# Kernel optimization log

Hardware: AMD Instinct MI355X
Metric: run time of the kernel (lower is better)

## Reference

```python
import jax, jax.numpy as jnp
import numpy as np

N = 50000      # num nodes
E = 400000     # num edges
D = 384        # input_dim
H = 4          # heads
C = 128        # hidden_dim per head
HC = H * C     # 512


def setup_inputs() -> dict:
    key = jax.random.key(0)
    ks = jax.random.split(key, 32)
    w = lambda k, shape: jax.random.normal(k, shape, jnp.float32) * 0.05
    inp = {
        "x": jax.random.normal(ks[0], (N, D), jnp.float32),
        "edge_index": jax.random.randint(ks[1], (2, E), 0, N, dtype=jnp.int32),
    }
    dims = [(D, HC), (HC, HC)]  # layer0 in=384, layer1 in=512
    i = 2
    for l, (din, dout) in enumerate(dims):
        for nm in ["q", "k", "v", "s"]:  # query/key/value/skip linears
            inp[f"{nm}{l}_w"] = w(ks[i], (dout, din)); i += 1
            inp[f"{nm}{l}_b"] = jnp.zeros((dout,), jnp.float32)
    inp["out_w"] = w(ks[i], (D, HC))
    inp["out_b"] = jnp.zeros((D,), jnp.float32)
    return inp


def _transformer_conv(x, src, dst, Wq, bq, Wk, bk, Wv, bv, Ws, bs):
    # PyG TransformerConv, concat=True, root_weight=True, no edge features.
    n = x.shape[0]
    q = (x @ Wq.T + bq).reshape(n, H, C)
    k = (x @ Wk.T + bk).reshape(n, H, C)
    v = (x @ Wv.T + bv).reshape(n, H, C)
    # per-edge attention logits [E, H]; target = dst, source = src
    alpha = (q[dst] * k[src]).sum(-1) / jnp.sqrt(jnp.float32(C))
    m = jax.ops.segment_max(alpha, dst, num_segments=n)
    m = jnp.where(jnp.isfinite(m), m, 0.0)  # nodes with no in-edges
    e = jnp.exp(alpha - m[dst])
    denom = jax.ops.segment_sum(e, dst, num_segments=n)
    a = e / (denom[dst] + 1e-16)             # segment softmax [E, H]
    msg = v[src] * a[:, :, None]             # [E, H, C]
    agg = jax.ops.segment_sum(msg, dst, num_segments=n).reshape(n, HC)
    return agg + x @ Ws.T + bs               # + root/skip connection


def reference(x, edge_index,
              q0_w, q0_b, k0_w, k0_b, v0_w, v0_b, s0_w, s0_b,
              q1_w, q1_b, k1_w, k1_b, v1_w, v1_b, s1_w, s1_b,
              out_w, out_b):
    src, dst = edge_index[0], edge_index[1]
    h = _transformer_conv(x, src, dst, q0_w, q0_b, k0_w, k0_b, v0_w, v0_b, s0_w, s0_b)
    h = jax.nn.relu(h)
    h = _transformer_conv(h, src, dst, q1_w, q1_b, k1_w, k1_b, v1_w, v1_b, s1_w, s1_b)
    h = jax.nn.relu(h)
    return h @ out_w.T + out_b  # [N, D]
```

## Files before the change

kernel.cpp:

```cpp
#include <hip/hip_runtime.h>
#include <hip/hip_bf16.h>

#define NN 50000
#define NE 400000
#define DD 384
#define HC 512

typedef unsigned int u32;
typedef unsigned short u16;
typedef __attribute__((ext_vector_type(8))) short bf16x8;
typedef __attribute__((ext_vector_type(4))) float f32x4;

#define AS1 __attribute__((address_space(1)))
#define AS3 __attribute__((address_space(3)))

__device__ __forceinline__ float bflo(u32 u){ return __uint_as_float(u << 16); }
__device__ __forceinline__ float bfhi(u32 u){ return __uint_as_float(u & 0xFFFF0000u); }
__device__ __forceinline__ u16 f2bf(float f){
    u32 u = __float_as_uint(f);
    return (u16)((u + 0x7FFFu + ((u >> 16) & 1u)) >> 16);
}
__device__ __forceinline__ u32 pack2(float a, float b){
    return (u32)f2bf(a) | ((u32)f2bf(b) << 16);
}
__device__ __forceinline__ float dot8(const float* q, uint4 k){
    return q[0] * bflo(k.x) + q[1] * bfhi(k.x)
         + q[2] * bflo(k.y) + q[3] * bfhi(k.y)
         + q[4] * bflo(k.z) + q[5] * bfhi(k.z)
         + q[6] * bflo(k.w) + q[7] * bfhi(k.w);
}

template<int K>
__global__ __launch_bounds__(512)
void gemm_ws(const u16* __restrict__ Ab, const u16* __restrict__ Wb,
             const float* __restrict__ bias,
             u16* __restrict__ oQ, u16* __restrict__ oK,
             u16* __restrict__ oV, u16* __restrict__ oS)
{
    constexpr int NKT  = K / 64;
    constexpr int WCH  = K / 8;
    constexpr int NPAN = (NN + 127) / 128;
    __shared__ char smW[128 * K * 2];
    __shared__ char smA[2][16384];

    const int b   = blockIdx.x;
    const int xcd = b & 7;
    const int idx = b >> 3;
    const int ct  = idx & 15;
    const int rh  = idx >> 4;

    const int tid  = threadIdx.x;
    const int lane = tid & 63;
    const int w    = tid >> 6;
    const int wq   = w >> 1;
    const int wc   = w & 1;
    const int r16  = lane & 15;
    const int kq   = lane >> 4;

    const u16* Wrow0 = Wb + (size_t)ct * 128 * K;
    #pragma unroll
    for (int p = 0; p < (128 * WCH) / 512; ++p) {
        int ci = p * 512 + tid;
        int row = ci / WCH, pc = ci % WCH;
        int lc = (pc & ~7) | ((pc ^ row) & 7);
        __builtin_amdgcn_global_load_lds((const AS1 u32*)(Wrow0 + (size_t)row * K + lc * 8),
                                         (AS3 u32*)(smW + (size_t)ci * 16), 16, 0, 0);
    }

    auto panel = [&](int j) { return (2 * j + rh) * 8 + xcd; };
    int np = 0;
    while (panel(np) < NPAN) ++np;
    const int total = np * NKT;

    auto stageA = [&](int t) {
        int j = t / NKT, kc = t - (t / NKT) * NKT;
        int m0 = panel(j) * 128;
        #pragma unroll
        for (int p = 0; p < 2; ++p) {
            int ci = p * 512 + tid;
            int row = ci >> 3, pc = ci & 7;
            int lc = pc ^ (row & 7);
            int gr = m0 + row; if (gr >= NN) gr = NN - 1;
            __builtin_amdgcn_global_load_lds((const AS1 u32*)(Ab + (size_t)gr * K + kc * 64 + lc * 8),
                                             (AS3 u32*)(smA[t & 1] + ci * 16), 16, 0, 0);
        }
    };

    stageA(0);
    stageA(1);

    f32x4 acc[2][4] = {};

    const int qsel = ct >> 2;
    u16* outp = (qsel == 0) ? oQ : (qsel == 1) ? oK : (qsel == 2) ? oV : oS;
    const int cb = (ct & 3) * 128 + wc * 64;
    float bv4[4];
    #pragma unroll
    for (int ni = 0; ni < 4; ++ni) bv4[ni] = bias[ct * 128 + wc * 64 + ni * 16 + r16];

    for (int t = 0; t < total; ++t) {
        if (t + 1 < total) { asm volatile("s_waitcnt vmcnt(2)" ::: "memory"); }
        else               { asm volatile("s_waitcnt vmcnt(0)" ::: "memory"); }
        __builtin_amdgcn_s_barrier();
        __builtin_amdgcn_sched_barrier(0);

        const int jj = t / NKT;
        const int kt = t - jj * NKT;
        const char* bufA = smA[t & 1];
        #pragma unroll
        for (int kk = 0; kk < 2; ++kk) {
            bf16x8 av[2], bv[4];
            #pragma unroll
            for (int i = 0; i < 2; ++i) {
                int rowA = wq * 32 + i * 16 + r16;
                int c = kk * 4 + kq;
                av[i] = *(const bf16x8*)(bufA + rowA * 128 + ((c ^ (rowA & 7)) << 4));
            }
            #pragma unroll
            for (int i = 0; i < 4; ++i) {
                int rowW = wc * 64 + i * 16 + r16;
                int c = kt * 8 + kk * 4 + kq;
                int pcw = (c & ~7) | ((c ^ rowW) & 7);
                bv[i] = *(const bf16x8*)(smW + (size_t)rowW * (K * 2) + (pcw << 4));
            }
            #pragma unroll
            for (int mi = 0; mi < 2; ++mi)
                #pragma unroll
                for (int ni = 0; ni < 4; ++ni)
                    acc[mi][ni] = __builtin_amdgcn_mfma_f32_16x16x32_bf16(
                        av[mi], bv[ni], acc[mi][ni], 0, 0, 0);
        }

        __builtin_amdgcn_sched_barrier(0);
        __builtin_amdgcn_s_barrier();
        __builtin_amdgcn_sched_barrier(0);

        if (kt == NKT - 1) {
            int m0 = panel(jj) * 128;
            #pragma unroll
            for (int ni = 0; ni < 4; ++ni) {
                int col = cb + ni * 16 + r16;
                float bb = bv4[ni];
                #pragma unroll
                for (int mi = 0; mi < 2; ++mi)
                    #pragma unroll
                    for (int r = 0; r < 4; ++r) {
                        int gr = m0 + wq * 32 + mi * 16 + kq * 4 + r;
                        if (gr < NN) outp[(size_t)gr * 512 + col] = f2bf(acc[mi][ni][r] + bb);
                        acc[mi][ni][r] = 0.f;
                    }
            }
        }
        if (t + 2 < total) stageA(t + 2);
    }
}

template<int K>
__global__ __launch_bounds__(256)
void gemm2ph(const u16* __restrict__ Ab, const u16* __restrict__ Wb,
             const float* __restrict__ bias, float* __restrict__ oF,
             int n, int Ototal, int NT)
{
    constexpr int NKT = K / 64;
    __shared__ char smA[2][16384];
    __shared__ char smB[2][16384];

    const int nb  = gridDim.x;
    const int bd  = blockIdx.x;
    const int q8  = nb >> 3, r8 = nb & 7;
    const int xcd = bd & 7, gg = bd >> 3;
    const int tt  = (xcd < r8 ? xcd * (q8 + 1) : r8 * (q8 + 1) + (xcd - r8) * q8) + gg;
    const int m0  = (tt / NT) * 128;
    const int o0  = (tt % NT) * 128;

    const int tid  = threadIdx.x;
    const int lane = tid & 63;
    const int w    = tid >> 6;
    const int wr   = w >> 1, wc = w & 1;
    const int r16  = lane & 15;
    const int kq   = lane >> 4;
    const int swz  = (r16 & 7) << 4;

    auto stage = [&](int bf, int kt) {
        #pragma unroll
        for (int p = 0; p < 4; ++p) {
            int ci = p * 256 + tid, row = ci >> 3, pc = ci & 7;
            int lc = pc ^ (row & 7);
            const u16* g = Wb + (size_t)(o0 + row) * K + kt * 64 + lc * 8;
            __builtin_amdgcn_global_load_lds((const AS1 u32*)g,
                                             (AS3 u32*)(smB[bf] + ci * 16), 16, 0, 0);
        }
        #pragma unroll
        for (int p = 0; p < 4; ++p) {
            int ci = p * 256 + tid, row = ci >> 3, pc = ci & 7;
            int lc = pc ^ (row & 7);
            int gr = m0 + row; if (gr >= n) gr = n - 1;
            const u16* g = Ab + (size_t)gr * K + kt * 64 + lc * 8;
            __builtin_amdgcn_global_load_lds((const AS1 u32*)g,
                                             (AS3 u32*)(smA[bf] + ci * 16), 16, 0, 0);
        }
    };

    f32x4 acc[4][4] = {};

    stage(0, 0);
    stage(1, 1);

    for (int kt = 0; kt < NKT; ++kt) {
        if (kt + 1 < NKT) { asm volatile("s_waitcnt vmcnt(8)" ::: "memory"); }
        else             { asm volatile("s_waitcnt vmcnt(0)" ::: "memory"); }
        __builtin_amdgcn_s_barrier();
        __builtin_amdgcn_sched_barrier(0);

        const char* pa = smA[kt & 1] + (wr * 64) * 128;
        const char* pb = smB[kt & 1] + (wc * 64) * 128;
        #pragma unroll
        for (int kk = 0; kk < 2; ++kk) {
            const int kb = kk * 64 + kq * 16;
            bf16x8 av[4], bv[4];
            #pragma unroll
            for (int i = 0; i < 4; ++i) {
                av[i] = *(const bf16x8*)(pa + (i * 16 + r16) * 128 + (kb ^ swz));
                bv[i] = *(const bf16x8*)(pb + (i * 16 + r16) * 128 + (kb ^ swz));
            }
            #pragma unroll
            for (int mi = 0; mi < 4; ++mi)
                #pragma unroll
                for (int ni = 0; ni < 4; ++ni)
                    acc[mi][ni] = __builtin_amdgcn_mfma_f32_16x16x32_bf16(
                        av[mi], bv[ni], acc[mi][ni], 0, 0, 0);
        }

        __builtin_amdgcn_sched_barrier(0);
        __builtin_amdgcn_s_barrier();
        __builtin_amdgcn_sched_barrier(0);
        if (kt + 2 < NKT) stage(kt & 1, kt + 2);
    }

    const int cbo = o0 + wc * 64;
    #pragma unroll
    for (int ni = 0; ni < 4; ++ni) {
        int col = cbo + ni * 16 + r16;
        float bb = bias[col];
        #pragma unroll
        for (int mi = 0; mi < 4; ++mi)
            #pragma unroll
            for (int r = 0; r < 4; ++r) {
                int gr = m0 + wr * 64 + mi * 16 + kq * 4 + r;
                if (gr < n) oF[(size_t)gr * Ototal + col] = acc[mi][ni][r] + bb;
            }
    }
}

#define XG  2400000
#define W0G 24576
#define W1G 32768
#define WOG 24576
#define CVT_TOTAL (XG + 4*W0G + 4*W1G + WOG)

__global__ __launch_bounds__(256)
void cvt_all(const float* __restrict__ x,
             const float* q0w, const float* k0w, const float* v0w, const float* s0w,
             const float* q1w, const float* k1w, const float* v1w, const float* s1w,
             const float* ow,
             u16* __restrict__ Xb, u16* __restrict__ Wc0,
             u16* __restrict__ Wc1, u16* __restrict__ WcO)
{
    int i = blockIdx.x * 256 + threadIdx.x;
    if (i >= CVT_TOTAL) return;
    const float* s; u16* d; int g;
    if (i < XG) { s = x; d = Xb; g = i; }
    else {
        int j = i - XG;
        if (j < 4 * W0G) {
            int q = j / W0G; g = j - q * W0G;
            s = (q == 0 ? q0w : q == 1 ? k0w : q == 2 ? v0w : s0w);
            d = Wc0 + (size_t)q * W0G * 8;
        } else if ((j -= 4 * W0G) < 4 * W1G) {
            int q = j / W1G; g = j - q * W1G;
            s = (q == 0 ? q1w : q == 1 ? k1w : q == 2 ? v1w : s1w);
            d = Wc1 + (size_t)q * W1G * 8;
        } else { j -= 4 * W1G; s = ow; d = WcO; g = j; }
    }
    float4 f0 = ((const float4*)s)[(size_t)g * 2];
    float4 f1 = ((const float4*)s)[(size_t)g * 2 + 1];
    uint4 o;
    o.x = pack2(f0.x, f0.y); o.y = pack2(f0.z, f0.w);
    o.z = pack2(f1.x, f1.y); o.w = pack2(f1.z, f1.w);
    ((uint4*)d)[g] = o;
}

__global__ __launch_bounds__(256)
void pack_bias(const float* q0, const float* k0, const float* v0, const float* s0,
               const float* q1, const float* k1, const float* v1, const float* s1,
               const float* ob, float* __restrict__ dst)
{
    int i = blockIdx.x * 256 + threadIdx.x;
    if (i >= 4480) return;
    float v;
    if (i < 2048) {
        int j = i & 511, q = i >> 9;
        v = (q == 0 ? q0 : q == 1 ? k0 : q == 2 ? v0 : s0)[j];
    } else if (i < 4096) {
        int j = i - 2048; int q = j >> 9; j &= 511;
        v = (q == 0 ? q1 : q == 1 ? k1 : q == 2 ? v1 : s1)[j];
    } else {
        v = ob[i - 4096];
    }
    dst[i] = v;
}

__global__ __launch_bounds__(256)
void zero_deg(int* __restrict__ deg)
{
    int i = blockIdx.x * 256 + threadIdx.x;
    if (i < NN) deg[i] = 0;
}

__global__ __launch_bounds__(256)
void hist_dst(const int* __restrict__ dst, int* __restrict__ deg)
{
    int e = blockIdx.x * 256 + threadIdx.x;
    if (e < NE) atomicAdd(&deg[dst[e]], 1);
}

__global__ __launch_bounds__(1024)
void scan_deg(const int* __restrict__ deg, int* __restrict__ rowptr,
              int* __restrict__ cursor)
{
    __shared__ int wsum[16];
    const int tid = threadIdx.x, lane = tid & 63, wid = tid >> 6;
    int carry = 0;
    for (int base = 0; base < NN; base += 1024) {
        int i = base + tid;
        int orig = (i < NN) ? deg[i] : 0;
        int v = orig;
        #pragma unroll
        for (int off = 1; off < 64; off <<= 1) {
            int t = __shfl_up(v, off, 64);
            if (lane >= off) v += t;
        }
        if (lane == 63) wsum[wid] = v;
        __syncthreads();
        if (wid == 0) {
            int s = (lane < 16) ? wsum[lane] : 0;
            #pragma unroll
            for (int off = 1; off < 16; off <<= 1) {
                int t = __shfl_up(s, off, 16);
                if ((lane & 15) >= off) s += t;
            }
            if (lane < 16) wsum[lane] = s;
        }
        __syncthreads();
        int woff  = (wid == 0) ? 0 : wsum[wid - 1];
        int total = wsum[15];
        int excl  = carry + woff + (v - orig);
        if (i < NN) { rowptr[i] = excl; cursor[i] = excl; }
        carry += total;
        __syncthreads();
    }
    if (tid == 0) rowptr[NN] = NE;
}

__global__ __launch_bounds__(256)
void scatter_edges(const int* __restrict__ src, const int* __restrict__ dst,
                   int* __restrict__ cursor, int* __restrict__ esrc_ord)
{
    int e = blockIdx.x * 256 + threadIdx.x;
    if (e >= NE) return;
    int pos = atomicAdd(&cursor[dst[e]], 1);
    esrc_ord[pos] = src[e];
}

__global__ __launch_bounds__(256)
void node_attn(const u16* __restrict__ Qb, const u16* __restrict__ Kb,
               const u16* __restrict__ Vb, const int* __restrict__ rowptr,
               const int* __restrict__ esrc, const u16* __restrict__ skipb,
               u16* __restrict__ outb)
{
    int d = blockIdx.x * 4 + (threadIdx.x >> 6);
    if (d >= NN) return;
    int lane = threadIdx.x & 63;

    uint4 qv = *((const uint4*)(Qb + (size_t)d * HC) + lane);
    float q[8] = { bflo(qv.x), bfhi(qv.x), bflo(qv.y), bfhi(qv.y),
                   bflo(qv.z), bfhi(qv.z), bflo(qv.w), bfhi(qv.w) };

    int beg = rowptr[d], end = rowptr[d + 1];
    int cnt = end - beg;
    float m = -INFINITY, den = 0.f;
    float acc[8] = {};

    uint4 k0, v0, k1, v1;
    if (cnt > 0) {
        int s = esrc[beg];
        k0 = *((const uint4*)(Kb + (size_t)s * HC) + lane);
        v0 = *((const uint4*)(Vb + (size_t)s * HC) + lane);
    }
    if (cnt > 1) {
        int s = esrc[beg + 1];
        k1 = *((const uint4*)(Kb + (size_t)s * HC) + lane);
        v1 = *((const uint4*)(Vb + (size_t)s * HC) + lane);
    }

    int i = beg;
    for (; i + 1 < end; i += 2) {
        uint4 ka = k0, va = v0, kb = k1, vb = v1;
        if (i + 2 < end) {
            int s = esrc[i + 2];
            k0 = *((const uint4*)(Kb + (size_t)s * HC) + lane);
            v0 = *((const uint4*)(Vb + (size_t)s * HC) + lane);
        }
        if (i + 3 < end) {
            int s = esrc[i + 3];
            k1 = *((const uint4*)(Kb + (size_t)s * HC) + lane);
            v1 = *((const uint4*)(Vb + (size_t)s * HC) + lane);
        }
        float s0 = dot8(q, ka);
        float s1 = dot8(q, kb);
        #pragma unroll
        for (int off = 1; off < 16; off <<= 1) {
            s0 += __shfl_xor(s0, off, 64);
            s1 += __shfl_xor(s1, off, 64);
        }
        float a0 = s0 * 0.08838834764831845f;
        float a1 = s1 * 0.08838834764831845f;

        float mnew  = fmaxf(m, fmaxf(a0, a1));
        float scale = __expf(m - mnew);
        float p0    = __expf(a0 - mnew);
        float p1    = __expf(a1 - mnew);
        den = den * scale + p0 + p1;

        acc[0] = acc[0] * scale + p0 * bflo(va.x) + p1 * bflo(vb.x);
        acc[1] = acc[1] * scale + p0 * bfhi(va.x) + p1 * bfhi(vb.x);
        acc[2] = acc[2] * scale + p0 * bflo(va.y) + p1 * bflo(vb.y);
        acc[3] = acc[3] * scale + p0 * bfhi(va.y) + p1 * bfhi(vb.y);
        acc[4] = acc[4] * scale + p0 * bflo(va.z) + p1 * bflo(vb.z);
        acc[5] = acc[5] * scale + p0 * bfhi(va.z) + p1 * bfhi(vb.z);
        acc[6] = acc[6] * scale + p0 * bflo(va.w) + p1 * bflo(vb.w);
        acc[7] = acc[7] * scale + p0 * bfhi(va.w) + p1 * bfhi(vb.w);
        m = mnew;
    }
    if (i < end) {
        float s0 = dot8(q, k0);
        #pragma unroll
        for (int off = 1; off < 16; off <<= 1) s0 += __shfl_xor(s0, off, 64);
        float a0 = s0 * 0.08838834764831845f;
        float mnew  = fmaxf(m, a0);
        float scale = __expf(m - mnew);
        float p0    = __expf(a0 - mnew);
        den = den * scale + p0;
        acc[0] = acc[0] * scale + p0 * bflo(v0.x);
        acc[1] = acc[1] * scale + p0 * bfhi(v0.x);
        acc[2] = acc[2] * scale + p0 * bflo(v0.y);
        acc[3] = acc[3] * scale + p0 * bfhi(v0.y);
        acc[4] = acc[4] * scale + p0 * bflo(v0.z);
        acc[5] = acc[5] * scale + p0 * bfhi(v0.z);
        acc[6] = acc[6] * scale + p0 * bflo(v0.w);
        acc[7] = acc[7] * scale + p0 * bfhi(v0.w);
    }

    float inv = 1.f / (den + 1e-16f);
    size_t base = (size_t)d * HC + lane * 8;
    uint4 sv = *((const uint4*)(skipb + base));
    float sk[8] = { bflo(sv.x), bfhi(sv.x), bflo(sv.y), bfhi(sv.y),
                    bflo(sv.z), bfhi(sv.z), bflo(sv.w), bfhi(sv.w) };
    uint4 o;
    o.x = pack2(fmaxf(acc[0] * inv + sk[0], 0.f), fmaxf(acc[1] * inv + sk[1], 0.f));
    o.y = pack2(fmaxf(acc[2] * inv + sk[2], 0.f), fmaxf(acc[3] * inv + sk[3], 0.f));
    o.z = pack2(fmaxf(acc[4] * inv + sk[4], 0.f), fmaxf(acc[5] * inv + sk[5], 0.f));
    o.w = pack2(fmaxf(acc[6] * inv + sk[6], 0.f), fmaxf(acc[7] * inv + sk[7], 0.f));
    *(uint4*)(outb + base) = o;
}

extern "C" void kernel_launch(void* const* d_in, const int* in_sizes, int n_in,
                              void* d_out, int out_size, void* d_ws, size_t ws_size,
                              hipStream_t stream)
{
    const float* x   = (const float*)d_in[0];
    const int* ei    = (const int*)d_in[1];
    const int* esrc  = ei;
    const int* edst  = ei + NE;
    const float* q0w = (const float*)d_in[2];  const float* q0b = (const float*)d_in[3];
    const float* k0w = (const float*)d_in[4];  const float* k0b = (const float*)d_in[5];
    const float* v0w = (const float*)d_in[6];  const float* v0b = (const float*)d_in[7];
    const float* s0w = (const float*)d_in[8];  const float* s0b = (const float*)d_in[9];
    const float* q1w = (const float*)d_in[10]; const float* q1b = (const float*)d_in[11];
    const float* k1w = (const float*)d_in[12]; const float* k1b = (const float*)d_in[13];
    const float* v1w = (const float*)d_in[14]; const float* v1b = (const float*)d_in[15];
    const float* s1w = (const float*)d_in[16]; const float* s1b = (const float*)d_in[17];
    const float* ow  = (const float*)d_in[18]; const float* obs = (const float*)d_in[19];

    char* p = (char*)d_ws;
    auto take = [&](size_t bytes) { void* r = (void*)p; p += (bytes + 255) & ~(size_t)255; return r; };
    u16*   Qb     = (u16*)take((size_t)NN * HC * 2);
    u16*   Vb     = (u16*)take((size_t)NN * HC * 2);
    u16*   Hb     = (u16*)take((size_t)NN * HC * 2);
    u16*   Sb     = (u16*)take((size_t)NN * HC * 2);
    u16*   Xb     = (u16*)take((size_t)NN * DD * 2);
    u16*   Wc0    = (u16*)take((size_t)2048 * DD * 2);
    u16*   Wc1    = (u16*)take((size_t)2048 * HC * 2);
    u16*   WcO    = (u16*)take((size_t)DD * HC * 2);
    float* barena = (float*)take(4480 * 4);

    char* dob = (char*)d_out;
    u16* Kb       = (u16*)dob;
    int* deg      = (int*)(dob + 51200000);
    int* rowptr   = (int*)(dob + 51400192);
    int* cursor   = (int*)(dob + 51600384);
    int* esrc_ord = (int*)(dob + 51800576);

    dim3 blk(256);
    int gN   = (NN + 255) / 256;
    int gE   = (NE + 255) / 256;
    int gnod = (NN + 3) / 4;
    const int NPAN = (NN + 127) / 128;
    int go = NPAN * 3;

    pack_bias<<<(4480 + 255) / 256, blk, 0, stream>>>(q0b, k0b, v0b, s0b,
                                                      q1b, k1b, v1b, s1b, obs, barena);
    cvt_all<<<(CVT_TOTAL + 255) / 256, blk, 0, stream>>>(x,
        q0w, k0w, v0w, s0w, q1w, k1w, v1w, s1w, ow, Xb, Wc0, Wc1, WcO);

    zero_deg      <<<gN, blk, 0, stream>>>(deg);
    hist_dst      <<<gE, blk, 0, stream>>>(edst, deg);
    scan_deg      <<<1, 1024, 0, stream>>>(deg, rowptr, cursor);
    scatter_edges <<<gE, blk, 0, stream>>>(esrc, edst, cursor, esrc_ord);

    gemm_ws<DD><<<256, 512, 0, stream>>>(Xb, Wc0, barena, Qb, Kb, Vb, Sb);
    node_attn<<<gnod, blk, 0, stream>>>(Qb, Kb, Vb, rowptr, esrc_ord, Sb, Hb);

    gemm_ws<HC><<<256, 512, 0, stream>>>(Hb, Wc1, barena + 2048, Qb, Kb, Vb, Sb);
    node_attn<<<gnod, blk, 0, stream>>>(Qb, Kb, Vb, rowptr, esrc_ord, Sb, Hb);

    gemm2ph<HC><<<go, blk, 0, stream>>>(Hb, WcO, barena + 4096,
                                        (float*)d_out, NN, 384, 3);
}
```

Baseline: 717.0 us.

## Deepen gather prefetch to four edges and reorder GEMM staging/waits

The node attention kernel now keeps four edges of K/V rows in flight instead of two. It issues the next K loads before the reductions and the next V loads after the accumulation, which hides more gather latency at the cost of more registers. The projection GEMM issues the next A-tile stage before the epilogue stores and relaxes the vmcnt wait around panel boundaries, so the stores overlap with the loads. The row bound check on stores is removed, and the output buffers are padded to 50048 rows to absorb the out-of-range rows, with the scratch offsets in the output buffer shifted to match.

```diff
diff --git a/kernel.cpp b/kernel.cpp
--- a/kernel.cpp
+++ b/kernel.cpp
@@ -2,6 +2,7 @@
 #include <hip/hip_bf16.h>
 
 #define NN 50000
+#define NP 50048
 #define NE 400000
 #define DD 384
 #define HC 512
@@ -99,13 +100,14 @@
     for (int ni = 0; ni < 4; ++ni) bv4[ni] = bias[ct * 128 + wc * 64 + ni * 16 + r16];
 
     for (int t = 0; t < total; ++t) {
-        if (t + 1 < total) { asm volatile("s_waitcnt vmcnt(2)" ::: "memory"); }
-        else               { asm volatile("s_waitcnt vmcnt(0)" ::: "memory"); }
+        const int jj = t / NKT;
+        const int kt = t - jj * NKT;
+        if (t + 1 >= total)          { asm volatile("s_waitcnt vmcnt(0)"  ::: "memory"); }
+        else if (t > 1 && kt <= 1)   { asm volatile("s_waitcnt vmcnt(34)" ::: "memory"); }
+        else                         { asm volatile("s_waitcnt vmcnt(2)"  ::: "memory"); }
         __builtin_amdgcn_s_barrier();
         __builtin_amdgcn_sched_barrier(0);
 
-        const int jj = t / NKT;
-        const int kt = t - jj * NKT;
         const char* bufA = smA[t & 1];
         #pragma unroll
         for (int kk = 0; kk < 2; ++kk) {
@@ -134,6 +136,8 @@
         __builtin_amdgcn_sched_barrier(0);
         __builtin_amdgcn_s_barrier();
         __builtin_amdgcn_sched_barrier(0);
+
+        if (t + 2 < total) stageA(t + 2);
 
         if (kt == NKT - 1) {
             int m0 = panel(jj) * 128;
@@ -146,12 +150,11 @@
                     #pragma unroll
                     for (int r = 0; r < 4; ++r) {
                         int gr = m0 + wq * 32 + mi * 16 + kq * 4 + r;
-                        if (gr < NN) outp[(size_t)gr * 512 + col] = f2bf(acc[mi][ni][r] + bb);
+                        outp[(size_t)gr * 512 + col] = f2bf(acc[mi][ni][r] + bb);
                         acc[mi][ni][r] = 0.f;
                     }
             }
         }
-        if (t + 2 < total) stageA(t + 2);
     }
 }
 
@@ -387,79 +390,89 @@
                    bflo(qv.z), bfhi(qv.z), bflo(qv.w), bfhi(qv.w) };
 
     int beg = rowptr[d], end = rowptr[d + 1];
-    int cnt = end - beg;
+    int n = end - beg;
     float m = -INFINITY, den = 0.f;
     float acc[8] = {};
 
-    uint4 k0, v0, k1, v1;
-    if (cnt > 0) {
-        int s = esrc[beg];
-        k0 = *((const uint4*)(Kb + (size_t)s * HC) + lane);
-        v0 = *((const uint4*)(Vb + (size_t)s * HC) + lane);
-    }
-    if (cnt > 1) {
-        int s = esrc[beg + 1];
-        k1 = *((const uint4*)(Kb + (size_t)s * HC) + lane);
-        v1 = *((const uint4*)(Vb + (size_t)s * HC) + lane);
-    }
+    uint4 k0, k1, k2, k3, v0, v1, v2, v3;
+    if (n > 0){ int s = esrc[beg];     k0 = *((const uint4*)(Kb + (size_t)s * HC) + lane);
+                                       v0 = *((const uint4*)(Vb + (size_t)s * HC) + lane); }
+    if (n > 1){ int s = esrc[beg + 1]; k1 = *((const uint4*)(Kb + (size_t)s * HC) + lane);
+                                       v1 = *((const uint4*)(Vb + (size_t)s * HC) + lane); }
+    if (n > 2){ int s = esrc[beg + 2]; k2 = *((const uint4*)(Kb + (size_t)s * HC) + lane);
+                                       v2 = *((const uint4*)(Vb + (size_t)s * HC) + lane); }
+    if (n > 3){ int s = esrc[beg + 3]; k3 = *((const uint4*)(Kb + (size_t)s * HC) + lane);
+                                       v3 = *((const uint4*)(Vb + (size_t)s * HC) + lane); }
+
+    auto single = [&](uint4 kk, uint4 vv){
+        float s0 = dot8(q, kk);
+        #pragma unroll
+        for (int off = 1; off < 16; off <<= 1) s0 += __shfl_xor(s0, off, 64);
+        float a0 = s0 * 0.08838834764831845f;
+        float mnew = fmaxf(m, a0);
+        float sc = __expf(m - mnew);
+        float p0 = __expf(a0 - mnew);
+        den = den * sc + p0;
+        acc[0] = acc[0] * sc + p0 * bflo(vv.x);
+        acc[1] = acc[1] * sc + p0 * bfhi(vv.x);
+        acc[2] = acc[2] * sc + p0 * bflo(vv.y);
+        acc[3] = acc[3] * sc + p0 * bfhi(vv.y);
+        acc[4] = acc[4] * sc + p0 * bflo(vv.z);
+        acc[5] = acc[5] * sc + p0 * bfhi(vv.z);
+        acc[6] = acc[6] * sc + p0 * bflo(vv.w);
+        acc[7] = acc[7] * sc + p0 * bfhi(vv.w);
+        m = mnew;
+    };
 
     int i = beg;
-    for (; i + 1 < end; i += 2) {
-        uint4 ka = k0, va = v0, kb = k1, vb = v1;
-        if (i + 2 < end) {
-            int s = esrc[i + 2];
-            k0 = *((const uint4*)(Kb + (size_t)s * HC) + lane);
-            v0 = *((const uint4*)(Vb + (size_t)s * HC) + lane);
-        }
-        if (i + 3 < end) {
-            int s = esrc[i + 3];
-            k1 = *((const uint4*)(Kb + (size_t)s * HC) + lane);
-            v1 = *((const uint4*)(Vb + (size_t)s * HC) + lane);
-        }
-        float s0 = dot8(q, ka);
-        float s1 = dot8(q, kb);
+    for (; i + 3 < end; i += 4) {
+        float s0 = dot8(q, k0), s1 = dot8(q, k1), s2 = dot8(q, k2), s3 = dot8(q, k3);
+        bool h0 = i + 4 < end, h1 = i + 5 < end, h2 = i + 6 < end, h3 = i + 7 < end;
+        int sn0 = 0, sn1 = 0, sn2 = 0, sn3 = 0;
+        if (h0) sn0 = esrc[i + 4];
+        if (h1) sn1 = esrc[i + 5];
+        if (h2) sn2 = esrc[i + 6];
+        if (h3) sn3 = esrc[i + 7];
+        if (h0) k0 = *((const uint4*)(Kb + (size_t)sn0 * HC) + lane);
+        if (h1) k1 = *((const uint4*)(Kb + (size_t)sn1 * HC) + lane);
+        if (h2) k2 = *((const uint4*)(Kb + (size_t)sn2 * HC) + lane);
+        if (h3) k3 = *((const uint4*)(Kb + (size_t)sn3 * HC) + lane);
         #pragma unroll
         for (int off = 1; off < 16; off <<= 1) {
             s0 += __shfl_xor(s0, off, 64);
             s1 += __shfl_xor(s1, off, 64);
+            s2 += __shfl_xor(s2, off, 64);
+            s3 += __shfl_xor(s3, off, 64);
         }
         float a0 = s0 * 0.08838834764831845f;
         float a1 = s1 * 0.08838834764831845f;
-
-        float mnew  = fmaxf(m, fmaxf(a0, a1));
-        float scale = __expf(m - mnew);
-        float p0    = __expf(a0 - mnew);
-        float p1    = __expf(a1 - mnew);
-        den = den * scale + p0 + p1;
-
-        acc[0] = acc[0] * scale + p0 * bflo(va.x) + p1 * bflo(vb.x);
-        acc[1] = acc[1] * scale + p0 * bfhi(va.x) + p1 * bfhi(vb.x);
-        acc[2] = acc[2] * scale + p0 * bflo(va.y) + p1 * bflo(vb.y);
-        acc[3] = acc[3] * scale + p0 * bfhi(va.y) + p1 * bfhi(vb.y);
-        acc[4] = acc[4] * scale + p0 * bflo(va.z) + p1 * bflo(vb.z);
-        acc[5] = acc[5] * scale + p0 * bfhi(va.z) + p1 * bfhi(vb.z);
-        acc[6] = acc[6] * scale + p0 * bflo(va.w) + p1 * bflo(vb.w);
-        acc[7] = acc[7] * scale + p0 * bfhi(va.w) + p1 * bfhi(vb.w);
+        float a2 = s2 * 0.08838834764831845f;
+        float a3 = s3 * 0.08838834764831845f;
+
+        float mnew = fmaxf(fmaxf(fmaxf(a0, a1), fmaxf(a2, a3)), m);
+        float sc = __expf(m - mnew);
+        float p0 = __expf(a0 - mnew), p1 = __expf(a1 - mnew);
+        float p2 = __expf(a2 - mnew), p3 = __expf(a3 - mnew);
+        den = den * sc + ((p0 + p1) + (p2 + p3));
+
+        acc[0] = acc[0] * sc + p0 * bflo(v0.x) + p1 * bflo(v1.x) + p2 * bflo(v2.x) + p3 * bflo(v3.x);
+        acc[1] = acc[1] * sc + p0 * bfhi(v0.x) + p1 * bfhi(v1.x) + p2 * bfhi(v2.x) + p3 * bfhi(v3.x);
+        acc[2] = acc[2] * sc + p0 * bflo(v0.y) + p1 * bflo(v1.y) + p2 * bflo(v2.y) + p3 * bflo(v3.y);
+        acc[3] = acc[3] * sc + p0 * bfhi(v0.y) + p1 * bfhi(v1.y) + p2 * bfhi(v2.y) + p3 * bfhi(v3.y);
+        acc[4] = acc[4] * sc + p0 * bflo(v0.z) + p1 * bflo(v1.z) + p2 * bflo(v2.z) + p3 * bflo(v3.z);
+        acc[5] = acc[5] * sc + p0 * bfhi(v0.z) + p1 * bfhi(v1.z) + p2 * bfhi(v2.z) + p3 * bfhi(v3.z);
+        acc[6] = acc[6] * sc + p0 * bflo(v0.w) + p1 * bflo(v1.w) + p2 * bflo(v2.w) + p3 * bflo(v3.w);
+        acc[7] = acc[7] * sc + p0 * bfhi(v0.w) + p1 * bfhi(v1.w) + p2 * bfhi(v2.w) + p3 * bfhi(v3.w);
         m = mnew;
-    }
-    if (i < end) {
-        float s0 = dot8(q, k0);
-        #pragma unroll
-        for (int off = 1; off < 16; off <<= 1) s0 += __shfl_xor(s0, off, 64);
-        float a0 = s0 * 0.08838834764831845f;
-        float mnew  = fmaxf(m, a0);
-        float scale = __expf(m - mnew);
-        float p0    = __expf(a0 - mnew);
-        den = den * scale + p0;
-        acc[0] = acc[0] * scale + p0 * bflo(v0.x);
-        acc[1] = acc[1] * scale + p0 * bfhi(v0.x);
-        acc[2] = acc[2] * scale + p0 * bflo(v0.y);
-        acc[3] = acc[3] * scale + p0 * bfhi(v0.y);
-        acc[4] = acc[4] * scale + p0 * bflo(v0.z);
-        acc[5] = acc[5] * scale + p0 * bfhi(v0.z);
-        acc[6] = acc[6] * scale + p0 * bflo(v0.w);
-        acc[7] = acc[7] * scale + p0 * bfhi(v0.w);
-    }
+
+        if (h0) v0 = *((const uint4*)(Vb + (size_t)sn0 * HC) + lane);
+        if (h1) v1 = *((const uint4*)(Vb + (size_t)sn1 * HC) + lane);
+        if (h2) v2 = *((const uint4*)(Vb + (size_t)sn2 * HC) + lane);
+        if (h3) v3 = *((const uint4*)(Vb + (size_t)sn3 * HC) + lane);
+    }
+    if (i < end)     single(k0, v0);
+    if (i + 1 < end) single(k1, v1);
+    if (i + 2 < end) single(k2, v2);
 
     float inv = 1.f / (den + 1e-16f);
     size_t base = (size_t)d * HC + lane * 8;
@@ -494,10 +507,10 @@
 
     char* p = (char*)d_ws;
     auto take = [&](size_t bytes) { void* r = (void*)p; p += (bytes + 255) & ~(size_t)255; return r; };
-    u16*   Qb     = (u16*)take((size_t)NN * HC * 2);
-    u16*   Vb     = (u16*)take((size_t)NN * HC * 2);
-    u16*   Hb     = (u16*)take((size_t)NN * HC * 2);
-    u16*   Sb     = (u16*)take((size_t)NN * HC * 2);
+    u16*   Qb     = (u16*)take((size_t)NP * HC * 2);
+    u16*   Vb     = (u16*)take((size_t)NP * HC * 2);
+    u16*   Hb     = (u16*)take((size_t)NP * HC * 2);
+    u16*   Sb     = (u16*)take((size_t)NP * HC * 2);
     u16*   Xb     = (u16*)take((size_t)NN * DD * 2);
     u16*   Wc0    = (u16*)take((size_t)2048 * DD * 2);
     u16*   Wc1    = (u16*)take((size_t)2048 * HC * 2);
@@ -506,10 +519,10 @@
 
     char* dob = (char*)d_out;
     u16* Kb       = (u16*)dob;
-    int* deg      = (int*)(dob + 51200000);
-    int* rowptr   = (int*)(dob + 51400192);
-    int* cursor   = (int*)(dob + 51600384);
-    int* esrc_ord = (int*)(dob + 51800576);
+    int* deg      = (int*)(dob + 51249152);
+    int* rowptr   = (int*)(dob + 51449344);
+    int* cursor   = (int*)(dob + 51649536);
+    int* esrc_ord = (int*)(dob + 51849728);
 
     dim3 blk(256);
     int gN   = (NN + 255) / 256;
```

After: 790.0 us. +10.2%, slower.

## Use persistent weight-stationary GEMM for output projection and vectorize degree scan

Applied to the files above, without the earlier changes.

Replaces the output-projection GEMM with a persistent kernel of 240 blocks. Each block loads a full 128-column slice of the output weight into LDS once, then streams row panels of activations through a double buffer and writes fp32 results per panel. This removes repeated reloads of the weight tiles and cuts launch tail effects, but it uses a large LDS footprint and spreads panels by a fixed XCD pattern. Separately, the degree prefix scan now processes four elements per thread with int4 loads, which reduces the number of serial block iterations.

```diff
diff --git a/kernel.cpp b/kernel.cpp
--- a/kernel.cpp
+++ b/kernel.cpp
@@ -155,76 +155,97 @@
     }
 }
 
-template<int K>
-__global__ __launch_bounds__(256)
-void gemm2ph(const u16* __restrict__ Ab, const u16* __restrict__ Wb,
-             const float* __restrict__ bias, float* __restrict__ oF,
-             int n, int Ototal, int NT)
-{
-    constexpr int NKT = K / 64;
+__global__ __launch_bounds__(512)
+void gemm_ws_f(const u16* __restrict__ Ab, const u16* __restrict__ Wb,
+               const float* __restrict__ bias, float* __restrict__ oF)
+{
+    constexpr int K    = 512;
+    constexpr int NKT  = 8;
+    constexpr int WCH  = 64;
+    constexpr int NPAN = (NN + 127) / 128;
+    __shared__ char smW[128 * K * 2];
     __shared__ char smA[2][16384];
-    __shared__ char smB[2][16384];
-
-    const int nb  = gridDim.x;
-    const int bd  = blockIdx.x;
-    const int q8  = nb >> 3, r8 = nb & 7;
-    const int xcd = bd & 7, gg = bd >> 3;
-    const int tt  = (xcd < r8 ? xcd * (q8 + 1) : r8 * (q8 + 1) + (xcd - r8) * q8) + gg;
-    const int m0  = (tt / NT) * 128;
-    const int o0  = (tt % NT) * 128;
+
+    const int b   = blockIdx.x;
+    const int xcd = b & 7;
+    const int idx = b >> 3;
+    const int ct  = idx % 3;
+    const int rh  = idx / 3;
 
     const int tid  = threadIdx.x;
     const int lane = tid & 63;
     const int w    = tid >> 6;
-    const int wr   = w >> 1, wc = w & 1;
+    const int wq   = w >> 1;
+    const int wc   = w & 1;
     const int r16  = lane & 15;
     const int kq   = lane >> 4;
-    const int swz  = (r16 & 7) << 4;
-
-    auto stage = [&](int bf, int kt) {
-        #pragma unroll
-        for (int p = 0; p < 4; ++p) {
-            int ci = p * 256 + tid, row = ci >> 3, pc = ci & 7;
+
+    const u16* Wrow0 = Wb + (size_t)ct * 128 * K;
+    #pragma unroll
+    for (int p = 0; p < (128 * WCH) / 512; ++p) {
+        int ci = p * 512 + tid;
+        int row = ci / WCH, pc = ci % WCH;
+        int lc = (pc & ~7) | ((pc ^ row) & 7);
+        __builtin_amdgcn_global_load_lds((const AS1 u32*)(Wrow0 + (size_t)row * K + lc * 8),
+                                         (AS3 u32*)(smW + (size_t)ci * 16), 16, 0, 0);
+    }
+
+    auto panel = [&](int j) { return (10 * j + rh) * 8 + xcd; };
+    int np = 0;
+    while (panel(np) < NPAN) ++np;
+    const int total = np * NKT;
+
+    auto stageA = [&](int t) {
+        int j = t / NKT, kc = t - (t / NKT) * NKT;
+        int m0 = panel(j) * 128;
+        #pragma unroll
+        for (int p = 0; p < 2; ++p) {
+            int ci = p * 512 + tid;
+            int row = ci >> 3, pc = ci & 7;
             int lc = pc ^ (row & 7);
-            const u16* g = Wb + (size_t)(o0 + row) * K + kt * 64 + lc * 8;
-            __builtin_amdgcn_global_load_lds((const AS1 u32*)g,
-                                             (AS3 u32*)(smB[bf] + ci * 16), 16, 0, 0);
-        }
-        #pragma unroll
-        for (int p = 0; p < 4; ++p) {
-            int ci = p * 256 + tid, row = ci >> 3, pc = ci & 7;
-            int lc = pc ^ (row & 7);
-            int gr = m0 + row; if (gr >= n) gr = n - 1;
-            const u16* g = Ab + (size_t)gr * K + kt * 64 + lc * 8;
-            __builtin_amdgcn_global_load_lds((const AS1 u32*)g,
-                                             (AS3 u32*)(smA[bf] + ci * 16), 16, 0, 0);
+            int gr = m0 + row; if (gr >= NN) gr = NN - 1;
+            __builtin_amdgcn_global_load_lds((const AS1 u32*)(Ab + (size_t)gr * K + kc * 64 + lc * 8),
+                                             (AS3 u32*)(smA[t & 1] + ci * 16), 16, 0, 0);
         }
     };
 
-    f32x4 acc[4][4] = {};
-
-    stage(0, 0);
-    stage(1, 1);
-
-    for (int kt = 0; kt < NKT; ++kt) {
-        if (kt + 1 < NKT) { asm volatile("s_waitcnt vmcnt(8)" ::: "memory"); }
-        else             { asm volatile("s_waitcnt vmcnt(0)" ::: "memory"); }
+    stageA(0);
+    stageA(1);
+
+    f32x4 acc[2][4] = {};
+
+    const int cb = ct * 128 + wc * 64;
+    float bv4[4];
+    #pragma unroll
+    for (int ni = 0; ni < 4; ++ni) bv4[ni] = bias[cb + ni * 16 + r16];
+
+    for (int t = 0; t < total; ++t) {
+        if (t + 1 < total) { asm volatile("s_waitcnt vmcnt(2)" ::: "memory"); }
+        else               { asm volatile("s_waitcnt vmcnt(0)" ::: "memory"); }
         __builtin_amdgcn_s_barrier();
         __builtin_amdgcn_sched_barrier(0);
 
-        const char* pa = smA[kt & 1] + (wr * 64) * 128;
-        const char* pb = smB[kt & 1] + (wc * 64) * 128;
+        const int jj = t / NKT;
+        const int kt = t - jj * NKT;
+        const char* bufA = smA[t & 1];
         #pragma unroll
         for (int kk = 0; kk < 2; ++kk) {
-            const int kb = kk * 64 + kq * 16;
-            bf16x8 av[4], bv[4];
+            bf16x8 av[2], bv[4];
+            #pragma unroll
+            for (int i = 0; i < 2; ++i) {
+                int rowA = wq * 32 + i * 16 + r16;
+                int c = kk * 4 + kq;
+                av[i] = *(const bf16x8*)(bufA + rowA * 128 + ((c ^ (rowA & 7)) << 4));
+            }
             #pragma unroll
             for (int i = 0; i < 4; ++i) {
-                av[i] = *(const bf16x8*)(pa + (i * 16 + r16) * 128 + (kb ^ swz));
-                bv[i] = *(const bf16x8*)(pb + (i * 16 + r16) * 128 + (kb ^ swz));
-            }
-            #pragma unroll
-            for (int mi = 0; mi < 4; ++mi)
+                int rowW = wc * 64 + i * 16 + r16;
+                int c = kt * 8 + kk * 4 + kq;
+                int pcw = (c & ~7) | ((c ^ rowW) & 7);
+                bv[i] = *(const bf16x8*)(smW + (size_t)rowW * (K * 2) + (pcw << 4));
+            }
+            #pragma unroll
+            for (int mi = 0; mi < 2; ++mi)
                 #pragma unroll
                 for (int ni = 0; ni < 4; ++ni)
                     acc[mi][ni] = __builtin_amdgcn_mfma_f32_16x16x32_bf16(
@@ -234,21 +255,24 @@
         __builtin_amdgcn_sched_barrier(0);
         __builtin_amdgcn_s_barrier();
         __builtin_amdgcn_sched_barrier(0);
-        if (kt + 2 < NKT) stage(kt & 1, kt + 2);
-    }
-
-    const int cbo = o0 + wc * 64;
-    #pragma unroll
-    for (int ni = 0; ni < 4; ++ni) {
-        int col = cbo + ni * 16 + r16;
-        float bb = bias[col];
-        #pragma unroll
-        for (int mi = 0; mi < 4; ++mi)
-            #pragma unroll
-            for (int r = 0; r < 4; ++r) {
-                int gr = m0 + wr * 64 + mi * 16 + kq * 4 + r;
-                if (gr < n) oF[(size_t)gr * Ototal + col] = acc[mi][ni][r] + bb;
-            }
+
+        if (kt == NKT - 1) {
+            int m0 = panel(jj) * 128;
+            #pragma unroll
+            for (int ni = 0; ni < 4; ++ni) {
+                int col = cb + ni * 16 + r16;
+                float bb = bv4[ni];
+                #pragma unroll
+                for (int mi = 0; mi < 2; ++mi)
+                    #pragma unroll
+                    for (int r = 0; r < 4; ++r) {
+                        int gr = m0 + wq * 32 + mi * 16 + kq * 4 + r;
+                        if (gr < NN) oF[(size_t)gr * 384 + col] = acc[mi][ni][r] + bb;
+                        acc[mi][ni][r] = 0.f;
+                    }
+            }
+        }
+        if (t + 2 < total) stageA(t + 2);
     }
 }
 
@@ -331,10 +355,17 @@
     __shared__ int wsum[16];
     const int tid = threadIdx.x, lane = tid & 63, wid = tid >> 6;
     int carry = 0;
-    for (int base = 0; base < NN; base += 1024) {
-        int i = base + tid;
-        int orig = (i < NN) ? deg[i] : 0;
-        int v = orig;
+    for (int base = 0; base < NN; base += 4096) {
+        int idx = base + tid * 4;
+        int4 v4 = make_int4(0, 0, 0, 0);
+        if (idx + 3 < NN)      v4 = *(const int4*)(deg + idx);
+        else if (idx < NN) {
+            v4.x = deg[idx];
+            if (idx + 1 < NN) v4.y = deg[idx + 1];
+            if (idx + 2 < NN) v4.z = deg[idx + 2];
+        }
+        int t0 = v4.x, t1 = t0 + v4.y, t2 = t1 + v4.z, t3 = t2 + v4.w;
+        int v = t3;
         #pragma unroll
         for (int off = 1; off < 64; off <<= 1) {
             int t = __shfl_up(v, off, 64);
@@ -354,8 +385,11 @@
         __syncthreads();
         int woff  = (wid == 0) ? 0 : wsum[wid - 1];
         int total = wsum[15];
-        int excl  = carry + woff + (v - orig);
-        if (i < NN) { rowptr[i] = excl; cursor[i] = excl; }
+        int texcl = carry + woff + (v - t3);
+        if (idx < NN)     { rowptr[idx]     = texcl;      cursor[idx]     = texcl; }
+        if (idx + 1 < NN) { rowptr[idx + 1] = texcl + t0; cursor[idx + 1] = texcl + t0; }
+        if (idx + 2 < NN) { rowptr[idx + 2] = texcl + t1; cursor[idx + 2] = texcl + t1; }
+        if (idx + 3 < NN) { rowptr[idx + 3] = texcl + t2; cursor[idx + 3] = texcl + t2; }
         carry += total;
         __syncthreads();
     }
@@ -515,8 +549,6 @@
     int gN   = (NN + 255) / 256;
     int gE   = (NE + 255) / 256;
     int gnod = (NN + 3) / 4;
-    const int NPAN = (NN + 127) / 128;
-    int go = NPAN * 3;
 
     pack_bias<<<(4480 + 255) / 256, blk, 0, stream>>>(q0b, k0b, v0b, s0b,
                                                       q1b, k1b, v1b, s1b, obs, barena);
@@ -534,6 +566,5 @@
     gemm_ws<HC><<<256, 512, 0, stream>>>(Hb, Wc1, barena + 2048, Qb, Kb, Vb, Sb);
     node_attn<<<gnod, blk, 0, stream>>>(Qb, Kb, Vb, rowptr, esrc_ord, Sb, Hb);
 
-    gemm2ph<HC><<<go, blk, 0, stream>>>(Hb, WcO, barena + 4096,
-                                        (float*)d_out, NN, 384, 3);
-}
+    gemm_ws_f<<<240, 512, 0, stream>>>(Hb, WcO, barena + 4096, (float*)d_out);
+}
```

New measurement: 673.2 us. 1.07x faster.
